# Optimization experiments

Hardware: AMD Instinct MI355X
Metric: run time of the kernel (lower is better)

Reference implementation:

```python
import jax, jax.numpy as jnp
import numpy as np

B, C, D, H, W = 4, 256, 16, 16, 16


def setup_inputs() -> dict:
    key = jax.random.key(0)
    ks = jax.random.split(key, 9)
    s = 1.0 / np.sqrt(C)
    inp = {
        "x": jax.random.normal(ks[0], (B, C, D, H, W), dtype=jnp.float32),
        "wq": jax.random.normal(ks[1], (C, C), dtype=jnp.float32) * s,
        "bq": jax.random.normal(ks[2], (C,), dtype=jnp.float32) * 0.02,
        "wk": jax.random.normal(ks[3], (C, C), dtype=jnp.float32) * s,
        "bk": jax.random.normal(ks[4], (C,), dtype=jnp.float32) * 0.02,
        "wv": jax.random.normal(ks[5], (C, C), dtype=jnp.float32) * s,
        "bv": jax.random.normal(ks[6], (C,), dtype=jnp.float32) * 0.02,
        "wp": jax.random.normal(ks[7], (C, C), dtype=jnp.float32) * s,
        "bp": jax.random.normal(ks[8], (C,), dtype=jnp.float32) * 0.02,
    }
    return inp


def reference(x, wq, bq, wk, bk, wv, bv, wp, bp):
    b, c, d, h, w = x.shape
    xf = x.reshape(b, c, d * h * w)  # (B, C, N)
    # 1x1 Conv3d == per-voxel linear map over channels
    q = jnp.einsum('oc,bcn->bon', wq, xf) + bq[:, None]
    k = jnp.einsum('oc,bcn->bon', wk, xf) + bk[:, None]
    v = jnp.einsum('oc,bcn->bon', wv, xf) + bv[:, None]
    # scores[b,i,j] = q[:, :, i] . k[:, :, j], scaled AFTER the bmm (as in source)
    scores = jnp.einsum('bci,bcj->bij', q, k) * (c ** -0.5)
    p = jax.nn.softmax(scores, axis=2)  # (B, N, N), softmax over keys j
    # attention[b,c,i] = sum_j v[b,c,j] * p[b,i,j]
    attn = jnp.einsum('bcj,bij->bci', v, p)
    out = jnp.einsum('oc,bcn->bon', wp, attn) + bp[:, None]
    return x + out.reshape(b, c, d, h, w)
```

## Files before the change

### kernel.cpp

```cpp
#include <hip/hip_runtime.h>

typedef unsigned short u16;
typedef unsigned int u32;
typedef __bf16 v8bf __attribute__((ext_vector_type(8)));
typedef float v4f __attribute__((ext_vector_type(4)));

#define DEV __device__ __forceinline__

constexpr int CB = 4;
constexpr int C = 256;
constexpr int NN = 4096;
constexpr float LOG2E = 1.4426950408889634f;
constexpr int PST = 44;

DEV u16 f2bf(float f) {
  union { float f; u32 u; } v; v.f = f;
  u32 r = v.u + 0x7fffu + ((v.u >> 16) & 1u);
  return (u16)(r >> 16);
}
DEV float bf2f(u16 h) {
  union { u32 u; float f; } v; v.u = ((u32)h) << 16; return v.f;
}

DEV void dma16(const u16* g, const u16* lds_base) {
  __builtin_amdgcn_global_load_lds(
      (const __attribute__((address_space(1))) void*)(unsigned long long)g,
      (__attribute__((address_space(3))) void*)(u32)(unsigned long long)lds_base,
      16, 0, 0);
}

__global__ __launch_bounds__(256) void k_transpose(const float* __restrict__ x,
                                                   u16* __restrict__ xT,
                                                   const float* __restrict__ wq,
                                                   const float* __restrict__ wk,
                                                   const float* __restrict__ wv,
                                                   const float* __restrict__ wp,
                                                   u16* __restrict__ wqb,
                                                   u16* __restrict__ wkb,
                                                   u16* __restrict__ wvb,
                                                   u16* __restrict__ wpb,
                                                   float* __restrict__ Mbuf) {
  __shared__ float tile[32][33];
  int b = blockIdx.z;
  if (b == 0) {
    int flat = blockIdx.x + 128 * blockIdx.y;
    if (flat == 0 && threadIdx.x < 8) Mbuf[threadIdx.x] = 0.f;
    if (flat < 1024) {
      int wsel = flat >> 8;
      const float* s = wsel == 0 ? wq : wsel == 1 ? wk : wsel == 2 ? wv : wp;
      u16* d = wsel == 0 ? wqb : wsel == 1 ? wkb : wsel == 2 ? wvb : wpb;
      int i = (flat & 255) * 256 + threadIdx.x;
      d[i] = f2bf(s[i]);
    }
  }
  int n0 = blockIdx.x * 32, c0 = blockIdx.y * 32;
  int tx = threadIdx.x & 31, ty = threadIdx.x >> 5;
  const float* xb = x + (long)b * C * NN;
#pragma unroll
  for (int r = 0; r < 4; ++r)
    tile[ty + r * 8][tx] = xb[(long)(c0 + ty + r * 8) * NN + n0 + tx];
  __syncthreads();
  u16* xTb = xT + (long)b * NN * C;
  int nl = threadIdx.x >> 3;
  int cseg = (threadIdx.x & 7) * 4;
  u16 ov[4];
#pragma unroll
  for (int j = 0; j < 4; ++j) ov[j] = f2bf(tile[cseg + j][nl]);
  *reinterpret_cast<uint2*>(&xTb[(long)(n0 + nl) * C + c0 + cseg]) =
      *reinterpret_cast<const uint2*>(ov);
}

DEV void stage_dma(const u16* __restrict__ g, const u16* lds, int w, int lane) {
#pragma unroll
  for (int i = 0; i < 8; ++i) {
    int idx = w * 8 + i;
    int r = idx * 2 + (lane >> 5);
    int cg = (lane & 31) ^ (r & 7);
    dma16(g + (long)r * 256 + cg * 8, lds + idx * 512);
  }
}

__global__ __launch_bounds__(256) void k_qkv(
    const u16* __restrict__ xT, const u16* __restrict__ wqb, const u16* __restrict__ wkb,
    const u16* __restrict__ wvb, const float* __restrict__ bq, const float* __restrict__ bk,
    const float* __restrict__ bv, u16* __restrict__ qO, u16* __restrict__ kO,
    u16* __restrict__ vO, float* __restrict__ Pn) {
  __shared__ __align__(16) u16 Ash[64 * 256];
  __shared__ __align__(16) u16 Bsh[64 * 256];
  __shared__ __align__(16) u16 QKb[64 * 72];
  int t = threadIdx.x, w = t >> 6, lane = t & 63, lr = lane & 15, q = lane >> 4;
  int m0 = blockIdx.x * 64, n0 = blockIdx.y * 64, b = blockIdx.z;
  const int xk = lr & 7;
  stage_dma(xT + (long)b * NN * C + (long)m0 * 256, Ash, w, lane);
  stage_dma(wqb + (long)n0 * 256, Bsh, w, lane);
  asm volatile("s_waitcnt vmcnt(0)\n\ts_barrier" ::: "memory");
#pragma unroll 1
  for (int wsel = 0; wsel < 3; ++wsel) {
    v4f acc[4];
#pragma unroll
    for (int nt = 0; nt < 4; ++nt)
#pragma unroll
      for (int r = 0; r < 4; ++r) acc[nt][r] = 0.f;
#pragma unroll
    for (int ks = 0; ks < 8; ++ks) {
      int cg = ((ks * 4 + q) ^ xk) << 3;
      v8bf a = *reinterpret_cast<const v8bf*>(Ash + (w * 16 + lr) * 256 + cg);
#pragma unroll
      for (int nt = 0; nt < 4; ++nt) {
        v8bf bb = *reinterpret_cast<const v8bf*>(Bsh + (nt * 16 + lr) * 256 + cg);
        acc[nt] = __builtin_amdgcn_mfma_f32_16x16x32_bf16(a, bb, acc[nt], 0, 0, 0);
      }
    }
    asm volatile("s_waitcnt lgkmcnt(0)\n\ts_barrier" ::: "memory");
    if (wsel < 2) {
      stage_dma((wsel == 0 ? wkb : wvb) + (long)n0 * 256, Bsh, w, lane);
      const float* bias = wsel == 0 ? bq : bk;
      float sn[4] = {0.f, 0.f, 0.f, 0.f};
#pragma unroll
      for (int nt = 0; nt < 4; ++nt) {
#pragma unroll
        for (int r = 0; r < 4; ++r) {
          int gn = n0 + nt * 16 + lr;
          float val = acc[nt][r] + bias[gn];
          u16 st;
          if (wsel == 0) {
            float vs = val * (0.0625f * LOG2E);
            st = f2bf(vs);
            sn[r] += vs * vs;
          } else {
            st = f2bf(val);
            sn[r] += val * val;
          }
          QKb[(w * 16 + q * 4 + r) * 72 + nt * 16 + lr] = st;
        }
      }
#pragma unroll
      for (int r = 0; r < 4; ++r) {
#pragma unroll
        for (int d = 1; d < 16; d <<= 1) sn[r] += __shfl_xor(sn[r], d, 64);
      }
      if (lr == 0) {
#pragma unroll
        for (int r = 0; r < 4; ++r)
          Pn[(((long)wsel * 4 + blockIdx.y) * CB + b) * NN + m0 + w * 16 + q * 4 + r] =
              sn[r];
      }
      asm volatile("s_waitcnt lgkmcnt(0)\n\ts_barrier" ::: "memory");
      {
        int gm_l = t >> 2, sg = (t & 3) * 16;
        u16* dst = (wsel == 0 ? qO : kO) + ((long)b * NN + m0 + gm_l) * C + n0 + sg;
        *reinterpret_cast<uint4*>(dst) =
            *reinterpret_cast<const uint4*>(QKb + gm_l * 72 + sg);
        *reinterpret_cast<uint4*>(dst + 8) =
            *reinterpret_cast<const uint4*>(QKb + gm_l * 72 + sg + 8);
      }
      asm volatile("s_waitcnt vmcnt(0)\n\ts_barrier" ::: "memory");
    } else {
      u16* Vt = Ash;
#pragma unroll
      for (int nt = 0; nt < 4; ++nt) {
#pragma unroll
        for (int r = 0; r < 4; ++r) {
          int gn_l = nt * 16 + lr;
          int gm_l = w * 16 + q * 4 + r;
          float val = acc[nt][r] + bv[n0 + gn_l];
          Vt[gn_l * 72 + gm_l] = f2bf(val);
        }
      }
      asm volatile("s_waitcnt lgkmcnt(0)\n\ts_barrier" ::: "memory");
      int row = t >> 2;
      u16* vrow = vO + (long)b * C * NN + (long)(n0 + row) * NN + m0;
#pragma unroll
      for (int s2 = 0; s2 < 2; ++s2) {
        int seg = (t & 3) * 2 + s2;
        *reinterpret_cast<uint4*>(vrow + seg * 8) =
            *reinterpret_cast<const uint4*>(Vt + row * 72 + seg * 8);
      }
    }
  }
}

__global__ __launch_bounds__(256) void k_norm(const float* __restrict__ Pn,
                                              float* __restrict__ Mbuf) {
  int tsel = blockIdx.y, b = blockIdx.z;
  float mx = 0.f;
  for (int row = threadIdx.x; row < NN; row += 256) {
    float s = 0.f;
#pragma unroll
    for (int qr = 0; qr < 4; ++qr)
      s += Pn[(((long)tsel * 4 + qr) * CB + b) * NN + row];
    mx = fmaxf(mx, s);
  }
#pragma unroll
  for (int d = 1; d < 64; d <<= 1) mx = fmaxf(mx, __shfl_xor(mx, d, 64));
  if ((threadIdx.x & 63) == 0)
    atomicMax((u32*)(Mbuf + tsel * 4 + b), __float_as_uint(mx));
}

DEV void kissue(const u16* kb, const u16* kshb, int j0, int w, int lane) {
#pragma unroll
  for (int i = 0; i < 4; ++i) {
    int idx = w * 4 + i;
    int kr = idx * 2 + (lane >> 5);
    int kc = (lane & 31) ^ (kr & 7);
    dma16(kb + (long)(j0 + kr) * 256 + kc * 8, kshb + idx * 512);
  }
}

#define FLASH_STEP(IT, VL, VU, PW, PR, KC, KN)                                     \
  {                                                                                \
    int jn_ = ((IT) + 1 < niter) ? jstart + (((IT) + 1) << 5) : jstart;            \
    kissue(kb, (KN), jn_, w, lane);                                                \
    asm volatile("" ::: "memory");    \
    {                                                                              \
      int jv_ = jstart + ((IT) << 5);                                              \
      _Pragma("unroll") for (int cs = 0; cs < 4; ++cs)                             \
          VL[cs] = *reinterpret_cast<const v8bf*>(                                 \
              vbw + (long)(cs * 16 + lr) * NN + jv_ + q * 8);                      \
    }                                                                              \
    v4f s0a_, s0b_, s1a_, s1b_;                                                    \
    _Pragma("unroll") for (int r = 0; r < 4; ++r) {                                \
      s0a_[r] = 0.f; s0b_[r] = 0.f; s1a_[r] = 0.f; s1b_[r] = 0.f;                  \
    }                                                                              \
    __builtin_amdgcn_s_setprio(1);                                                 \
    _Pragma("unroll") for (int ks = 0; ks < 4; ++ks) {                             \
      int cgA_ = ((ks * 4 + q) ^ xk) << 3;                                         \
      int cgB_ = (((ks + 4) * 4 + q) ^ xk) << 3;                                   \
      v8bf k0a_ = *reinterpret_cast<const v8bf*>((KC) + lr * 256 + cgA_);          \
      v8bf k1a_ = *reinterpret_cast<const v8bf*>((KC) + (16 + lr) * 256 + cgA_);   \
      v8bf k0b_ = *reinterpret_cast<const v8bf*>((KC) + lr * 256 + cgB_);          \
      v8bf k1b_ = *reinterpret_cast<const v8bf*>((KC) + (16 + lr) * 256 + cgB_);   \
      s0a_ = __builtin_amdgcn_mfma_f32_16x16x32_bf16(qf[ks], k0a_, s0a_, 0, 0, 0); \
      s1a_ = __builtin_amdgcn_mfma_f32_16x16x32_bf16(qf[ks], k1a_, s1a_, 0, 0, 0); \
      s0b_ = __builtin_amdgcn_mfma_f32_16x16x32_bf16(qf[ks + 4], k0b_, s0b_, 0, 0, 0); \
      s1b_ = __builtin_amdgcn_mfma_f32_16x16x32_bf16(qf[ks + 4], k1b_, s1b_, 0, 0, 0); \
    }                                                                              \
    __builtin_amdgcn_s_setprio(0);                                                 \
    v4f s0_ = s0a_ + s0b_;                                                         \
    v4f s1_ = s1a_ + s1b_;                                                         \
    _Pragma("unroll") for (int r = 0; r < 4; ++r) {                                \
      float p0_ = exp2f(s0_[r] - M);                                               \
      float p1_ = exp2f(s1_[r] - M);                                               \
      lsum[r] += p0_ + p1_;                                                        \
      (PW)[(q * 4 + r) * PST + lr] = (u16)((__float_as_uint(p0_) + 0x8000u) >> 16);\
      (PW)[(q * 4 + r) * PST + 16 + lr] =                                          \
          (u16)((__float_as_uint(p1_) + 0x8000u) >> 16);                           \
    }                                                                              \
    if ((IT) > 0) {                                                                \
      v8bf pa_[4];                                                                 \
      _Pragma("unroll") for (int qs = 0; qs < 4; ++qs)                             \
          pa_[qs] = *reinterpret_cast<const v8bf*>(                                \
              (PR) + (qs * 16 + lr) * PST + q * 8);                                \
      __builtin_amdgcn_s_setprio(1);                                               \
      _Pragma("unroll") for (int cs = 0; cs < 4; ++cs)                             \
        _Pragma("unroll") for (int qs = 0; qs < 4; ++qs)                           \
          accO[qs * 4 + cs] = __builtin_amdgcn_mfma_f32_16x16x32_bf16(             \
              pa_[qs], VU[cs], accO[qs * 4 + cs], 0, 0, 0);                        \
      __builtin_amdgcn_s_setprio(0);                                               \
    }                                                                              \
    asm volatile("s_waitcnt vmcnt(4) lgkmcnt(0)\n\ts_barrier" ::: "memory");       \
  }

__global__ __launch_bounds__(256, 2) void k_flash(const u16* __restrict__ qT,
                                                  const u16* __restrict__ kT,
                                                  const u16* __restrict__ V,
                                                  u16* __restrict__ op0,
                                                  u16* __restrict__ op1,
                                                  float* __restrict__ ml,
                                                  const float* __restrict__ Mbuf,
                                                  int span) {
  __shared__ __align__(16) u16 ksh[2][32 * 256];
  __shared__ __align__(16) u16 psh[2][64 * PST];
  int t = threadIdx.x;
  int w = t >> 6, lane = t & 63, lr = lane & 15, q = lane >> 4;
  int total = gridDim.x * gridDim.y * gridDim.z;
  int flat = blockIdx.x + gridDim.x * (blockIdx.y + gridDim.y * blockIdx.z);
  int nf = (flat & 7) * (total >> 3) + (flat >> 3);
  int h = (nf >> 6) & (gridDim.y - 1);
  int b = nf >> (6 + __builtin_ctz(gridDim.y));
  int i0 = (nf & 63) * 64;
  const u16* qb = qT + ((long)b * NN + i0 + w * 16) * C;
  const u16* kb = kT + (long)b * NN * C;
  const u16* vbw = V + (long)b * C * NN + (long)(w * 64) * NN;
  float M = sqrtf(Mbuf[b] * Mbuf[4 + b]) + 1.5f;

  v8bf qf[8];
#pragma unroll
  for (int ks = 0; ks < 8; ++ks)
    qf[ks] = *reinterpret_cast<const v8bf*>(qb + lr * C + ks * 32 + q * 8);

  v4f accO[16];
#pragma unroll
  for (int ct = 0; ct < 16; ++ct)
#pragma unroll
    for (int r = 0; r < 4; ++r) accO[ct][r] = 0.f;
  float lsum[4] = {0.f, 0.f, 0.f, 0.f};

  u16* pw0 = psh[0] + w * 16 * PST;
  u16* pw1 = psh[1] + w * 16 * PST;
  const int xk = lr & 7;

  int jstart = h * span;
  int niter = span >> 5;

  kissue(kb, ksh[0], jstart, w, lane);
  asm volatile("s_waitcnt vmcnt(0)\n\ts_barrier" ::: "memory");

  v8bf vA[4] = {}, vB[4] = {};
#pragma unroll 1
  for (int it2 = 0; it2 < niter; it2 += 2) {
    FLASH_STEP(it2,     vA, vB, pw0, psh[1], ksh[0], ksh[1])
    FLASH_STEP(it2 + 1, vB, vA, pw1, psh[0], ksh[1], ksh[0])
  }
  {
    v8bf pa_[4];
#pragma unroll
    for (int qs = 0; qs < 4; ++qs)
      pa_[qs] = *reinterpret_cast<const v8bf*>(psh[1] + (qs * 16 + lr) * PST + q * 8);
#pragma unroll
    for (int cs = 0; cs < 4; ++cs)
#pragma unroll
      for (int qs = 0; qs < 4; ++qs)
        accO[qs * 4 + cs] = __builtin_amdgcn_mfma_f32_16x16x32_bf16(
            pa_[qs], vB[cs], accO[qs * 4 + cs], 0, 0, 0);
  }

#pragma unroll
  for (int r = 0; r < 4; ++r) {
#pragma unroll
    for (int d = 1; d < 16; d <<= 1) lsum[r] += __shfl_xor(lsum[r], d, 64);
  }
  u16* opp = h == 0 ? op0 : op1;
  u16* ob = opp + ((long)b * NN + i0) * C;
#pragma unroll
  for (int qs = 0; qs < 4; ++qs)
#pragma unroll
    for (int cs = 0; cs < 4; ++cs)
#pragma unroll
      for (int r = 0; r < 4; ++r)
        ob[(qs * 16 + q * 4 + r) * C + w * 64 + cs * 16 + lr] =
            f2bf(accO[qs * 4 + cs][r]);
  if (lr == 0) {
    long rbase = ((long)h * CB + b) * NN + i0 + w * 16 + q * 4;
#pragma unroll
    for (int r = 0; r < 4; ++r) {
      ml[(rbase + r) * 2] = M;
      ml[(rbase + r) * 2 + 1] = lsum[r];
    }
  }
}

__global__ __launch_bounds__(256) void k_gemmC(
    const u16* __restrict__ wpb, const u16* __restrict__ p0, const u16* __restrict__ p1,
    const float* __restrict__ ml, const float* __restrict__ bp,
    const float* __restrict__ x, float* __restrict__ out) {
  __shared__ __align__(16) u16 Ash[64 * 256];
  __shared__ __align__(16) u16 Bsh[64 * 256];
  int t = threadIdx.x;
  int w = t >> 6, lane = t & 63, lr = lane & 15, q = lane >> 4;
  int m0 = blockIdx.x * 64, n0 = blockIdx.y * 64, b = blockIdx.z;
  const int xk = lr & 7;
  const long nc = (long)NN * C;
  stage_dma(wpb + (long)m0 * 256, Ash, w, lane);
#pragma unroll
  for (int i = 0; i < 8; ++i) {
    int idx = w * 8 + i;
    int r = idx * 2 + (lane >> 5);
    int cg = (lane & 31) ^ (r & 7);
    long goff = (long)b * nc + (long)(n0 + r) * 256 + cg * 8;
    uint4 u0 = *reinterpret_cast<const uint4*>(p0 + goff);
    uint4 u1 = *reinterpret_cast<const uint4*>(p1 + goff);
    float l0 = ml[(((long)0 * CB + b) * NN + n0 + r) * 2 + 1];
    float l1 = ml[(((long)1 * CB + b) * NN + n0 + r) * 2 + 1];
    float inv = 1.0f / (l0 + l1);
    const u16* e0 = reinterpret_cast<const u16*>(&u0);
    const u16* e1 = reinterpret_cast<const u16*>(&u1);
    u16 cv[8];
#pragma unroll
    for (int k2 = 0; k2 < 8; ++k2)
      cv[k2] = f2bf((bf2f(e0[k2]) + bf2f(e1[k2])) * inv);
    *reinterpret_cast<uint4*>(Bsh + idx * 512 + lane * 8) =
        *reinterpret_cast<const uint4*>(cv);
  }
  asm volatile("s_waitcnt vmcnt(0) lgkmcnt(0)\n\ts_barrier" ::: "memory");
  v4f acc[4];
#pragma unroll
  for (int nt = 0; nt < 4; ++nt)
#pragma unroll
    for (int r = 0; r < 4; ++r) acc[nt][r] = 0.f;
#pragma unroll
  for (int ks = 0; ks < 8; ++ks) {
    int cg = ((ks * 4 + q) ^ xk) << 3;
    v8bf a = *reinterpret_cast<const v8bf*>(Ash + (w * 16 + lr) * 256 + cg);
#pragma unroll
    for (int nt = 0; nt < 4; ++nt) {
      v8bf bb = *reinterpret_cast<const v8bf*>(Bsh + (nt * 16 + lr) * 256 + cg);
      acc[nt] = __builtin_amdgcn_mfma_f32_16x16x32_bf16(a, bb, acc[nt], 0, 0, 0);
    }
  }
  asm volatile("s_waitcnt lgkmcnt(0)\n\ts_barrier" ::: "memory");
  float* Of = reinterpret_cast<float*>(Ash);
#pragma unroll
  for (int nt = 0; nt < 4; ++nt)
#pragma unroll
    for (int r = 0; r < 4; ++r)
      Of[(w * 16 + q * 4 + r) * 68 + nt * 16 + lr] = acc[nt][r];
  asm volatile("s_waitcnt lgkmcnt(0)\n\ts_barrier" ::: "memory");
  {
    int gm_l = t >> 2, sg = (t & 3) * 16;
    long rowa = (long)b * nc + (long)(m0 + gm_l) * NN + n0 + sg;
    float bpv = bp[m0 + gm_l];
#pragma unroll
    for (int j4 = 0; j4 < 4; ++j4) {
      float4 ov = *reinterpret_cast<const float4*>(&Of[gm_l * 68 + sg + j4 * 4]);
      float4 xv = *reinterpret_cast<const float4*>(&x[rowa + j4 * 4]);
      float4 res;
      res.x = ov.x + bpv + xv.x;
      res.y = ov.y + bpv + xv.y;
      res.z = ov.z + bpv + xv.z;
      res.w = ov.w + bpv + xv.w;
      *reinterpret_cast<float4*>(&out[rowa + j4 * 4]) = res;
    }
  }
}

extern "C" void kernel_launch(void* const* d_in, const int* in_sizes, int n_in,
                              void* d_out, int out_size, void* d_ws, size_t ws_size,
                              hipStream_t stream) {
  const float* x = (const float*)d_in[0];
  const float* wq = (const float*)d_in[1];
  const float* bq = (const float*)d_in[2];
  const float* wk = (const float*)d_in[3];
  const float* bk = (const float*)d_in[4];
  const float* wv = (const float*)d_in[5];
  const float* bv = (const float*)d_in[6];
  const float* wp = (const float*)d_in[7];
  const float* bp = (const float*)d_in[8];
  float* out = (float*)d_out;
  char* ws = (char*)d_ws;

  const long SLOT = 8388608L;

  u16* wqb = (u16*)(ws + 0);
  u16* wkb = (u16*)(ws + 131072L);
  u16* wvb = (u16*)(ws + 262144L);
  u16* wpb = (u16*)(ws + 393216L);
  char* base = ws + 524288L;
  u16* xT  = (u16*)(base);
  u16* qTw = (u16*)(base + 1 * SLOT);
  u16* kTw = (u16*)(base + 2 * SLOT);
  u16* vw  = (u16*)(base + 3 * SLOT);
  u16* op1 = (u16*)(base + 4 * SLOT);
  float* ml = (float*)(base + 5 * SLOT);
  float* Mbuf = ml + 131072;
  u16* op0 = xT;
  float* Pn = (float*)op1;

  k_transpose<<<dim3(128, 8, CB), 256, 0, stream>>>(x, xT, wq, wk, wv, wp, wqb, wkb,
                                                    wvb, wpb, Mbuf);
  k_qkv<<<dim3(64, 4, CB), 256, 0, stream>>>(xT, wqb, wkb, wvb, bq, bk, bv, qTw, kTw,
                                             vw, Pn);
  k_norm<<<dim3(1, 2, CB), 256, 0, stream>>>(Pn, Mbuf);
  k_flash<<<dim3(64, 2, CB), 256, 0, stream>>>(qTw, kTw, vw, op0, op1, ml, Mbuf,
                                               NN / 2);
  k_gemmC<<<dim3(4, 64, CB), 256, 0, stream>>>(wpb, op0, op1, ml, bp, x, out);
}
```

Baseline: 231.6 us.

## Split flash attention across eight waves per block by key and channel halves

The flash kernel grows from 4 to 8 waves per block. Wave pairs now split each 32-key tile, so each wave computes 16 score columns, and the PV product is split so each wave owns 32 output channels. Per-row softmax partial sums from the two key halves are combined through a small shared array before being written. The aim is more waves per CU for latency hiding and fewer accumulator registers per wave. The cost is an extra barrier, duplicated Q fragment loads, and smaller MFMA batches per wave between barriers.

```diff
diff --git a/kernel.cpp b/kernel.cpp
--- a/kernel.cpp
+++ b/kernel.cpp
@@ -197,54 +197,44 @@
     atomicMax((u32*)(Mbuf + tsel * 4 + b), __float_as_uint(mx));
 }
 
-DEV void kissue(const u16* kb, const u16* kshb, int j0, int w, int lane) {
-#pragma unroll
-  for (int i = 0; i < 4; ++i) {
-    int idx = w * 4 + i;
+DEV void kissue8(const u16* kb, const u16* kshb, int j0, int w, int lane) {
+#pragma unroll
+  for (int i = 0; i < 2; ++i) {
+    int idx = w * 2 + i;
     int kr = idx * 2 + (lane >> 5);
     int kc = (lane & 31) ^ (kr & 7);
     dma16(kb + (long)(j0 + kr) * 256 + kc * 8, kshb + idx * 512);
   }
 }
 
-#define FLASH_STEP(IT, VL, VU, PW, PR, KC, KN)                                     \
+#define FLASH_STEP8(IT, VL, VU, PW, PR, KC, KN)                                    \
   {                                                                                \
     int jn_ = ((IT) + 1 < niter) ? jstart + (((IT) + 1) << 5) : jstart;            \
-    kissue(kb, (KN), jn_, w, lane);                                                \
+    kissue8(kb, (KN), jn_, w, lane);                                               \
     asm volatile("" ::: "memory");    \
     {                                                                              \
       int jv_ = jstart + ((IT) << 5);                                              \
-      _Pragma("unroll") for (int cs = 0; cs < 4; ++cs)                             \
+      _Pragma("unroll") for (int cs = 0; cs < 2; ++cs)                             \
           VL[cs] = *reinterpret_cast<const v8bf*>(                                 \
               vbw + (long)(cs * 16 + lr) * NN + jv_ + q * 8);                      \
     }                                                                              \
-    v4f s0a_, s0b_, s1a_, s1b_;                                                    \
-    _Pragma("unroll") for (int r = 0; r < 4; ++r) {                                \
-      s0a_[r] = 0.f; s0b_[r] = 0.f; s1a_[r] = 0.f; s1b_[r] = 0.f;                  \
-    }                                                                              \
+    v4f sa_, sb_;                                                                  \
+    _Pragma("unroll") for (int r = 0; r < 4; ++r) { sa_[r] = 0.f; sb_[r] = 0.f; }  \
     __builtin_amdgcn_s_setprio(1);                                                 \
     _Pragma("unroll") for (int ks = 0; ks < 4; ++ks) {                             \
       int cgA_ = ((ks * 4 + q) ^ xk) << 3;                                         \
       int cgB_ = (((ks + 4) * 4 + q) ^ xk) << 3;                                   \
-      v8bf k0a_ = *reinterpret_cast<const v8bf*>((KC) + lr * 256 + cgA_);          \
-      v8bf k1a_ = *reinterpret_cast<const v8bf*>((KC) + (16 + lr) * 256 + cgA_);   \
-      v8bf k0b_ = *reinterpret_cast<const v8bf*>((KC) + lr * 256 + cgB_);          \
-      v8bf k1b_ = *reinterpret_cast<const v8bf*>((KC) + (16 + lr) * 256 + cgB_);   \
-      s0a_ = __builtin_amdgcn_mfma_f32_16x16x32_bf16(qf[ks], k0a_, s0a_, 0, 0, 0); \
-      s1a_ = __builtin_amdgcn_mfma_f32_16x16x32_bf16(qf[ks], k1a_, s1a_, 0, 0, 0); \
-      s0b_ = __builtin_amdgcn_mfma_f32_16x16x32_bf16(qf[ks + 4], k0b_, s0b_, 0, 0, 0); \
-      s1b_ = __builtin_amdgcn_mfma_f32_16x16x32_bf16(qf[ks + 4], k1b_, s1b_, 0, 0, 0); \
+      v8bf ka_ = *reinterpret_cast<const v8bf*>((KC) + krow * 256 + cgA_);         \
+      v8bf kb_ = *reinterpret_cast<const v8bf*>((KC) + krow * 256 + cgB_);         \
+      sa_ = __builtin_amdgcn_mfma_f32_16x16x32_bf16(qf[ks], ka_, sa_, 0, 0, 0);    \
+      sb_ = __builtin_amdgcn_mfma_f32_16x16x32_bf16(qf[ks + 4], kb_, sb_, 0, 0, 0);\
     }                                                                              \
     __builtin_amdgcn_s_setprio(0);                                                 \
-    v4f s0_ = s0a_ + s0b_;                                                         \
-    v4f s1_ = s1a_ + s1b_;                                                         \
+    v4f s_ = sa_ + sb_;                                                            \
     _Pragma("unroll") for (int r = 0; r < 4; ++r) {                                \
-      float p0_ = exp2f(s0_[r] - M);                                               \
-      float p1_ = exp2f(s1_[r] - M);                                               \
-      lsum[r] += p0_ + p1_;                                                        \
-      (PW)[(q * 4 + r) * PST + lr] = (u16)((__float_as_uint(p0_) + 0x8000u) >> 16);\
-      (PW)[(q * 4 + r) * PST + 16 + lr] =                                          \
-          (u16)((__float_as_uint(p1_) + 0x8000u) >> 16);                           \
+      float p_ = exp2f(s_[r] - M);                                                 \
+      lsum[r] += p_;                                                               \
+      (PW)[(q * 4 + r) * PST + lr] = (u16)((__float_as_uint(p_) + 0x8000u) >> 16); \
     }                                                                              \
     if ((IT) > 0) {                                                                \
       v8bf pa_[4];                                                                 \
@@ -252,16 +242,16 @@
           pa_[qs] = *reinterpret_cast<const v8bf*>(                                \
               (PR) + (qs * 16 + lr) * PST + q * 8);                                \
       __builtin_amdgcn_s_setprio(1);                                               \
-      _Pragma("unroll") for (int cs = 0; cs < 4; ++cs)                             \
+      _Pragma("unroll") for (int cs = 0; cs < 2; ++cs)                             \
         _Pragma("unroll") for (int qs = 0; qs < 4; ++qs)                           \
-          accO[qs * 4 + cs] = __builtin_amdgcn_mfma_f32_16x16x32_bf16(             \
-              pa_[qs], VU[cs], accO[qs * 4 + cs], 0, 0, 0);                        \
+          accO[qs * 2 + cs] = __builtin_amdgcn_mfma_f32_16x16x32_bf16(             \
+              pa_[qs], VU[cs], accO[qs * 2 + cs], 0, 0, 0);                        \
       __builtin_amdgcn_s_setprio(0);                                               \
     }                                                                              \
-    asm volatile("s_waitcnt vmcnt(4) lgkmcnt(0)\n\ts_barrier" ::: "memory");       \
-  }
-
-__global__ __launch_bounds__(256, 2) void k_flash(const u16* __restrict__ qT,
+    asm volatile("s_waitcnt vmcnt(2) lgkmcnt(0)\n\ts_barrier" ::: "memory");       \
+  }
+
+__global__ __launch_bounds__(512, 4) void k_flash(const u16* __restrict__ qT,
                                                   const u16* __restrict__ kT,
                                                   const u16* __restrict__ V,
                                                   u16* __restrict__ op0,
@@ -271,17 +261,19 @@
                                                   int span) {
   __shared__ __align__(16) u16 ksh[2][32 * 256];
   __shared__ __align__(16) u16 psh[2][64 * PST];
+  __shared__ float lsh[8][16];
   int t = threadIdx.x;
   int w = t >> 6, lane = t & 63, lr = lane & 15, q = lane >> 4;
+  int wr = w & 3, wj = w >> 2;
   int total = gridDim.x * gridDim.y * gridDim.z;
   int flat = blockIdx.x + gridDim.x * (blockIdx.y + gridDim.y * blockIdx.z);
   int nf = (flat & 7) * (total >> 3) + (flat >> 3);
   int h = (nf >> 6) & (gridDim.y - 1);
   int b = nf >> (6 + __builtin_ctz(gridDim.y));
   int i0 = (nf & 63) * 64;
-  const u16* qb = qT + ((long)b * NN + i0 + w * 16) * C;
+  const u16* qb = qT + ((long)b * NN + i0 + wr * 16) * C;
   const u16* kb = kT + (long)b * NN * C;
-  const u16* vbw = V + (long)b * C * NN + (long)(w * 64) * NN;
+  const u16* vbw = V + (long)b * C * NN + (long)(w * 32) * NN;
   float M = sqrtf(Mbuf[b] * Mbuf[4 + b]) + 1.5f;
 
   v8bf qf[8];
@@ -289,28 +281,29 @@
   for (int ks = 0; ks < 8; ++ks)
     qf[ks] = *reinterpret_cast<const v8bf*>(qb + lr * C + ks * 32 + q * 8);
 
-  v4f accO[16];
-#pragma unroll
-  for (int ct = 0; ct < 16; ++ct)
+  v4f accO[8];
+#pragma unroll
+  for (int ct = 0; ct < 8; ++ct)
 #pragma unroll
     for (int r = 0; r < 4; ++r) accO[ct][r] = 0.f;
   float lsum[4] = {0.f, 0.f, 0.f, 0.f};
 
-  u16* pw0 = psh[0] + w * 16 * PST;
-  u16* pw1 = psh[1] + w * 16 * PST;
+  u16* pw0 = psh[0] + (wr * 16) * PST + wj * 16;
+  u16* pw1 = psh[1] + (wr * 16) * PST + wj * 16;
   const int xk = lr & 7;
+  const int krow = wj * 16 + lr;
 
   int jstart = h * span;
   int niter = span >> 5;
 
-  kissue(kb, ksh[0], jstart, w, lane);
+  kissue8(kb, ksh[0], jstart, w, lane);
   asm volatile("s_waitcnt vmcnt(0)\n\ts_barrier" ::: "memory");
 
-  v8bf vA[4] = {}, vB[4] = {};
+  v8bf vA[2] = {}, vB[2] = {};
 #pragma unroll 1
   for (int it2 = 0; it2 < niter; it2 += 2) {
-    FLASH_STEP(it2,     vA, vB, pw0, psh[1], ksh[0], ksh[1])
-    FLASH_STEP(it2 + 1, vB, vA, pw1, psh[0], ksh[1], ksh[0])
+    FLASH_STEP8(it2,     vA, vB, pw0, psh[1], ksh[0], ksh[1])
+    FLASH_STEP8(it2 + 1, vB, vA, pw1, psh[0], ksh[1], ksh[0])
   }
   {
     v8bf pa_[4];
@@ -318,11 +311,11 @@
     for (int qs = 0; qs < 4; ++qs)
       pa_[qs] = *reinterpret_cast<const v8bf*>(psh[1] + (qs * 16 + lr) * PST + q * 8);
 #pragma unroll
-    for (int cs = 0; cs < 4; ++cs)
+    for (int cs = 0; cs < 2; ++cs)
 #pragma unroll
       for (int qs = 0; qs < 4; ++qs)
-        accO[qs * 4 + cs] = __builtin_amdgcn_mfma_f32_16x16x32_bf16(
-            pa_[qs], vB[cs], accO[qs * 4 + cs], 0, 0, 0);
+        accO[qs * 2 + cs] = __builtin_amdgcn_mfma_f32_16x16x32_bf16(
+            pa_[qs], vB[cs], accO[qs * 2 + cs], 0, 0, 0);
   }
 
 #pragma unroll
@@ -330,22 +323,28 @@
 #pragma unroll
     for (int d = 1; d < 16; d <<= 1) lsum[r] += __shfl_xor(lsum[r], d, 64);
   }
+  if (lr == 0) {
+#pragma unroll
+    for (int r = 0; r < 4; ++r) lsh[w][q * 4 + r] = lsum[r];
+  }
+  asm volatile("s_waitcnt lgkmcnt(0)\n\ts_barrier" ::: "memory");
+
   u16* opp = h == 0 ? op0 : op1;
   u16* ob = opp + ((long)b * NN + i0) * C;
 #pragma unroll
   for (int qs = 0; qs < 4; ++qs)
 #pragma unroll
-    for (int cs = 0; cs < 4; ++cs)
+    for (int cs = 0; cs < 2; ++cs)
 #pragma unroll
       for (int r = 0; r < 4; ++r)
-        ob[(qs * 16 + q * 4 + r) * C + w * 64 + cs * 16 + lr] =
-            f2bf(accO[qs * 4 + cs][r]);
-  if (lr == 0) {
+        ob[(qs * 16 + q * 4 + r) * C + w * 32 + cs * 16 + lr] =
+            f2bf(accO[qs * 2 + cs][r]);
+  if (w < 4 && lr == 0) {
     long rbase = ((long)h * CB + b) * NN + i0 + w * 16 + q * 4;
 #pragma unroll
     for (int r = 0; r < 4; ++r) {
       ml[(rbase + r) * 2] = M;
-      ml[(rbase + r) * 2 + 1] = lsum[r];
+      ml[(rbase + r) * 2 + 1] = lsh[w][q * 4 + r] + lsh[w + 4][q * 4 + r];
     }
   }
 }
@@ -461,7 +460,7 @@
   k_qkv<<<dim3(64, 4, CB), 256, 0, stream>>>(xT, wqb, wkb, wvb, bq, bk, bv, qTw, kTw,
                                              vw, Pn);
   k_norm<<<dim3(1, 2, CB), 256, 0, stream>>>(Pn, Mbuf);
-  k_flash<<<dim3(64, 2, CB), 256, 0, stream>>>(qTw, kTw, vw, op0, op1, ml, Mbuf,
+  k_flash<<<dim3(64, 2, CB), 512, 0, stream>>>(qTw, kTw, vw, op0, op1, ml, Mbuf,
                                                NN / 2);
   k_gemmC<<<dim3(4, 64, CB), 256, 0, stream>>>(wpb, op0, op1, ml, bp, x, out);
 }
```

Measured after the change: 273.5 us. 18.1% more time.
